# Kernel tuning notes

Hardware: AMD Instinct MI355X
Metric: run time of the kernel (lower is better)

The kernel has to match this reference:

```python
import jax, jax.numpy as jnp
import numpy as np
import math

B, T, WIDTH, NUM_HEADS, WINDOW = 2, 2048, 1024, 16, 1024
HEAD_DIM = WIDTH // NUM_HEADS
_MIN_LOGITS_VALUE = -1e30


def setup_inputs() -> dict:
    key = jax.random.key(0)
    k1, k2, k3, k4, k5 = jax.random.split(key, 5)
    std = math.sqrt(1.0 / WIDTH)
    x = jax.random.normal(k1, (B, T, WIDTH), dtype=jnp.float32)
    segment_pos = jnp.tile(jnp.arange(T, dtype=jnp.int32)[None, :], (B, 1))
    Wq = jax.random.normal(k2, (WIDTH, WIDTH), dtype=jnp.float32) * std
    Wk = jax.random.normal(k3, (HEAD_DIM, WIDTH), dtype=jnp.float32) * std
    Wv = jax.random.normal(k4, (HEAD_DIM, WIDTH), dtype=jnp.float32) * std
    Wf = jax.random.normal(k5, (WIDTH, WIDTH), dtype=jnp.float32) * std
    bf = jnp.zeros((WIDTH,), dtype=jnp.float32)
    return {"x": x, "segment_pos": segment_pos, "Wq": Wq, "Wk": Wk, "Wv": Wv, "Wf": Wf, "bf": bf}


def reference(x, segment_pos, Wq, Wk, Wv, Wf, bf):
    b, t, _ = x.shape
    # projections (torch Linear: y = x @ W.T)
    q = (x @ Wq.T).reshape(b, t, NUM_HEADS, HEAD_DIM)  # b t n h
    k = x @ Wk.T  # b s h  (single shared KV head, MQA)
    v = x @ Wv.T  # b s h
    scale = 1.0 / math.sqrt(HEAD_DIM)
    logits = jnp.einsum('btnh,bsh->bnts', q, k) * scale
    pos = jnp.arange(t)
    q_pos = pos[:, None]
    k_pos = pos[None, :]
    mask = (q_pos >= k_pos) & (q_pos <= k_pos + WINDOW)  # [t, t]
    masked = jnp.where(mask[None, None, :, :], logits, _MIN_LOGITS_VALUE)
    probs = jax.nn.softmax(masked.astype(jnp.float32), axis=-1).astype(logits.dtype)
    out = jnp.einsum('bnts,bsh->btnh', probs, v).reshape(b, t, WIDTH)
    return out @ Wf.T + bf
```

## Files before the change

kernel.cpp:

```cpp
#include <hip/hip_runtime.h>
#include <cstdint>
#include <cstddef>

#define BB      2
#define TT      2048
#define WID     1024
#define NH      16
#define HD      64
#define WIN     1024
#define MROWS   (BB*TT)
#define NQKV    1152
#define QSCL    0.18033688011112042f

typedef __attribute__((ext_vector_type(8))) short  short8;
typedef __attribute__((ext_vector_type(4))) float  floatx4;

__device__ __forceinline__ unsigned short f2bf(float f) {
  union { float f; unsigned int u; } v; v.f = f;
  unsigned int u = v.u;
  unsigned int r = (u + 0x7fffu + ((u >> 16) & 1u)) >> 16;
  return (unsigned short)r;
}

__device__ __forceinline__ float fast_exp2(float x) {
#if __has_builtin(__builtin_amdgcn_exp2f)
  return __builtin_amdgcn_exp2f(x);
#else
  return exp2f(x);
#endif
}

__device__ __forceinline__ unsigned int pk_bf16_trunc(float lo, float hi) {
  union { float f; unsigned int u; } a, b; a.f = lo; b.f = hi;
#if __has_builtin(__builtin_amdgcn_perm)
  return __builtin_amdgcn_perm(b.u, a.u, 0x07060302u);
#else
  return (b.u & 0xffff0000u) | (a.u >> 16);
#endif
}

__device__ __forceinline__ void gld_lds16(const void* g, void* l) {
  __builtin_amdgcn_global_load_lds(
      (const __attribute__((address_space(1))) unsigned int*)g,
      (__attribute__((address_space(3))) unsigned int*)l, 16, 0, 0);
}

__global__ __launch_bounds__(256) void convert_kernel(
    const float* __restrict__ x,  const float* __restrict__ wq,
    const float* __restrict__ wk, const float* __restrict__ wv,
    const float* __restrict__ wf,
    unsigned short* __restrict__ xb, unsigned short* __restrict__ wb,
    unsigned short* __restrict__ wfb)
{
  const int NX4 = (MROWS * WID) / 4;
  const int NQ4 = (WID * WID) / 4;
  const int NK4 = (HD * WID) / 4;
  const int NW4 = NQ4 + 2 * NK4;
  const int NF4 = (WID * WID) / 4;
  const int TOT = NX4 + NW4 + NF4;
  for (int i = blockIdx.x * blockDim.x + threadIdx.x; i < TOT;
       i += gridDim.x * blockDim.x) {
    float4 v4;
    unsigned short* dptr;
    if (i < NX4) {
      v4 = ((const float4*)x)[i];
      dptr = xb + (size_t)i * 4;
    } else if (i < NX4 + NW4) {
      int k = i - NX4;
      dptr = wb + (size_t)k * 4;
      if (k < NQ4)            v4 = ((const float4*)wq)[k];
      else if (k < NQ4 + NK4) v4 = ((const float4*)wk)[k - NQ4];
      else                    v4 = ((const float4*)wv)[k - NQ4 - NK4];
    } else {
      int k = i - NX4 - NW4;
      v4 = ((const float4*)wf)[k];
      dptr = wfb + (size_t)k * 4;
    }
    ushort4 o4 = make_ushort4(f2bf(v4.x), f2bf(v4.y), f2bf(v4.z), f2bf(v4.w));
    *(ushort4*)dptr = o4;
  }
}

__global__ __launch_bounds__(256) void gemm64(
    const unsigned short* __restrict__ A, const unsigned short* __restrict__ Bm,
    int M, int N, int K, int mode,
    float* __restrict__ C, const float* __restrict__ bias,
    unsigned short* __restrict__ qb, unsigned short* __restrict__ kb,
    unsigned short* __restrict__ vtb)
{
  __shared__ __align__(16) unsigned short As[2][64 * 64];
  __shared__ __align__(16) unsigned short Bs[2][128 * 64];

  const int tid  = threadIdx.x;
  const int m0   = blockIdx.x * 64;
  const int n0   = blockIdx.y * 128;
  const int w    = tid >> 6;
  const int lane = tid & 63;
  const int wr   = w >> 1;
  const int wc   = w & 1;
  const int quad = lane >> 4;
  const int l16  = lane & 15;

  const int rS  = tid >> 3;
  const int cS  = tid & 7;
  const int csS = (cS + rS) & 7;
  const unsigned short* gA0 = A  + (size_t)(m0 + rS) * K + csS * 8;
  const unsigned short* gA1 = gA0 + (size_t)32 * K;
  const unsigned short* gB0 = Bm + (size_t)(n0 + rS) * K + csS * 8;
  const unsigned short* gB1 = gB0 + (size_t)32 * K;
  const unsigned short* gB2 = gB0 + (size_t)64 * K;
  const unsigned short* gB3 = gB0 + (size_t)96 * K;
  const int wub = (tid & 192) * 16;

  floatx4 acc[2][4];
#pragma unroll
  for (int it = 0; it < 2; ++it)
#pragma unroll
    for (int jt = 0; jt < 4; ++jt)
      acc[it][jt] = (floatx4){0.f, 0.f, 0.f, 0.f};

  const int K64 = K >> 6;
  gld_lds16(gA0, (char*)As[0] + wub);
  gld_lds16(gA1, (char*)As[0] + 4096 + wub);
  gld_lds16(gB0, (char*)Bs[0] + wub);
  gld_lds16(gB1, (char*)Bs[0] + 4096 + wub);
  gld_lds16(gB2, (char*)Bs[0] + 8192 + wub);
  gld_lds16(gB3, (char*)Bs[0] + 12288 + wub);
  __syncthreads();

  for (int kt = 0; kt < K64; ++kt) {
    const int cur = kt & 1;
    if (kt + 1 < K64) {
      const int nxt = cur ^ 1;
      const int off = (kt + 1) * 64;
      gld_lds16(gA0 + off, (char*)As[nxt] + wub);
      gld_lds16(gA1 + off, (char*)As[nxt] + 4096 + wub);
      gld_lds16(gB0 + off, (char*)Bs[nxt] + wub);
      gld_lds16(gB1 + off, (char*)Bs[nxt] + 4096 + wub);
      gld_lds16(gB2 + off, (char*)Bs[nxt] + 8192 + wub);
      gld_lds16(gB3 + off, (char*)Bs[nxt] + 12288 + wub);
    }
    const unsigned short* as = As[cur];
    const unsigned short* bs = Bs[cur];
    short8 af[2][2], bfr[4][2];
#pragma unroll
    for (int it = 0; it < 2; ++it) {
      const int m = wr * 32 + it * 16 + l16;
#pragma unroll
      for (int ks = 0; ks < 2; ++ks)
        af[it][ks] = *(const short8*)(as + m * 64 + (((ks * 4 + quad) - m) & 7) * 8);
    }
#pragma unroll
    for (int jt = 0; jt < 4; ++jt) {
      const int n = wc * 64 + jt * 16 + l16;
#pragma unroll
      for (int ks = 0; ks < 2; ++ks)
        bfr[jt][ks] = *(const short8*)(bs + n * 64 + (((ks * 4 + quad) - n) & 7) * 8);
    }
#pragma unroll
    for (int ks = 0; ks < 2; ++ks)
#pragma unroll
      for (int it = 0; it < 2; ++it)
#pragma unroll
        for (int jt = 0; jt < 4; ++jt)
          acc[it][jt] = __builtin_amdgcn_mfma_f32_16x16x32_bf16(
              af[it][ks], bfr[jt][ks], acc[it][jt], 0, 0, 0);
    __syncthreads();
  }

  if (mode == 0) {
#pragma unroll
    for (int it = 0; it < 2; ++it) {
      const int gr = m0 + wr * 32 + it * 16 + quad * 4;
#pragma unroll
      for (int jt = 0; jt < 4; ++jt) {
        const int gc = n0 + wc * 64 + jt * 16 + l16;
        const float badd = bias[gc];
#pragma unroll
        for (int r = 0; r < 4; ++r)
          C[(size_t)(gr + r) * N + gc] = acc[it][jt][r] + badd;
      }
    }
  } else {
#pragma unroll
    for (int it = 0; it < 2; ++it) {
      const int gr = m0 + wr * 32 + it * 16 + quad * 4;
#pragma unroll
      for (int jt = 0; jt < 4; ++jt) {
        const int gc = n0 + wc * 64 + jt * 16 + l16;
        if (gc < WID) {
#pragma unroll
          for (int r = 0; r < 4; ++r)
            qb[(size_t)(gr + r) * WID + gc] = f2bf(acc[it][jt][r] * QSCL);
        } else if (gc < WID + HD) {
#pragma unroll
          for (int r = 0; r < 4; ++r)
            kb[(size_t)(gr + r) * HD + (gc - WID)] = f2bf(acc[it][jt][r]);
        } else {
          ushort4 o4 = make_ushort4(f2bf(acc[it][jt][0]), f2bf(acc[it][jt][1]),
                                    f2bf(acc[it][jt][2]), f2bf(acc[it][jt][3]));
          *(ushort4*)(vtb + (size_t)(gc - WID - HD) * MROWS + gr) = o4;
        }
      }
    }
  }
}

__global__ __launch_bounds__(512) void attn_mfma(
    const unsigned short* __restrict__ qb, const unsigned short* __restrict__ kb,
    const unsigned short* __restrict__ vtb, unsigned short* __restrict__ attnb)
{
  __shared__ __align__(16) unsigned short smem[30720];

  const int tid  = threadIdx.x;
  const int w    = tid >> 6;
  const int g    = w >> 2;
  const int wh   = w & 3;
  const int lane = tid & 63;
  const int l16  = lane & 15;
  const int quad = lane >> 4;
  const int t0   = blockIdx.x * 32;
  const int h    = blockIdx.y * 4 + wh;
  const int b    = blockIdx.z;

  unsigned short* Psb = smem + 20480 + w * 1280;

  short8 qf[2][2];
#pragma unroll
  for (int nt = 0; nt < 2; ++nt) {
    const unsigned short* qp =
        qb + (size_t)(b * TT + t0 + nt * 16 + l16) * WID + h * HD + quad * 8;
    qf[nt][0] = *(const short8*)qp;
    qf[nt][1] = *(const short8*)(qp + 32);
  }

  floatx4 Oacc[4][2];
#pragma unroll
  for (int mh = 0; mh < 4; ++mh)
#pragma unroll
    for (int nt = 0; nt < 2; ++nt)
      Oacc[mh][nt] = (floatx4){0.f, 0.f, 0.f, 0.f};
  float lq[2] = {0.f, 0.f};

  int s_begin = t0 - WIN; if (s_begin < 0) s_begin = 0;
  const int T = ((t0 + 32) - s_begin) >> 5;
  const int I = (T + 1) >> 1;

  const int kkey  = tid >> 3;
  const int khseg = (tid & 7) * 8;
  const int ksel  = kkey >> 5, krow = kkey & 31;
  const int vhd   = tid >> 3;
  const int vkk   = (tid & 7) * 8;
  const int vsel  = vkk >> 5,  vcol = vkk & 31;

  const unsigned short* kbase = kb  + (size_t)(b * TT) * HD;
  const unsigned short* vbase = vtb + (size_t)vhd * MROWS + b * TT;

  int s0p = s_begin;
  int ck = s0p + kkey; if (ck > TT - 1) ck = TT - 1;
  int cv = s0p + vkk;  if (cv > TT - 8) cv = TT - 8;
  short8 kreg = *(const short8*)(kbase + (size_t)ck * HD + khseg);
  short8 vreg = *(const short8*)(vbase + cv);

  for (int i = 0; i < I; ++i) {
    const int buf = i & 1;
    *(short8*)(smem + buf * 5120 + ksel * 2560 + krow * 80 + khseg) = kreg;
    *(short8*)(smem + 10240 + buf * 5120 + vsel * 2560 + vhd * 40 + vcol) = vreg;
    __syncthreads();
    if (i + 1 < I) {
      s0p += 64;
      ck = s0p + kkey; if (ck > TT - 1) ck = TT - 1;
      cv = s0p + vkk;  if (cv > TT - 8) cv = TT - 8;
      kreg = *(const short8*)(kbase + (size_t)ck * HD + khseg);
      vreg = *(const short8*)(vbase + cv);
    }

    const int ta = 2 * i + g;
    if (ta < T) {
      const int s0 = s_begin + ta * 32;
      const unsigned short* ks = smem + buf * 5120 + g * 2560;
      const unsigned short* vs = smem + 10240 + buf * 5120 + g * 2560;

      short8 kf[2][2];
#pragma unroll
      for (int mk = 0; mk < 2; ++mk)
#pragma unroll
        for (int k2 = 0; k2 < 2; ++k2)
          kf[mk][k2] = *(const short8*)(ks + (mk * 16 + l16) * 80 + k2 * 32 + quad * 8);

      floatx4 Sc[2][2];
#pragma unroll
      for (int mk = 0; mk < 2; ++mk)
#pragma unroll
        for (int nt = 0; nt < 2; ++nt)
          Sc[mk][nt] = (floatx4){0.f, 0.f, 0.f, 0.f};
#pragma unroll
      for (int mk = 0; mk < 2; ++mk)
#pragma unroll
        for (int nt = 0; nt < 2; ++nt)
#pragma unroll
          for (int k2 = 0; k2 < 2; ++k2)
            Sc[mk][nt] = __builtin_amdgcn_mfma_f32_16x16x32_bf16(
                kf[mk][k2], qf[nt][k2], Sc[mk][nt], 0, 0, 0);

      const int mode = (s0 == t0) ? 2 : ((t0 >= WIN && s0 == t0 - WIN) ? 1 : 0);

#pragma unroll
      for (int nt = 0; nt < 2; ++nt) {
        const int t = t0 + nt * 16 + l16;
        float p[8], ps = 0.f;
#pragma unroll
        for (int mk = 0; mk < 2; ++mk)
#pragma unroll
          for (int r = 0; r < 4; ++r) {
            float v = Sc[mk][nt][r];
            if (mode) {
              const int s = s0 + mk * 16 + quad * 4 + r;
              const bool kill = (mode == 2) ? (s > t) : (s + WIN < t);
              if (kill) v = -1.0e5f;
            }
            const float e = fast_exp2(v);
            p[mk * 4 + r] = e; ps += e;
          }
        lq[nt] += ps;
        uint2 w0 = make_uint2(pk_bf16_trunc(p[0], p[1]), pk_bf16_trunc(p[2], p[3]));
        uint2 w1 = make_uint2(pk_bf16_trunc(p[4], p[5]), pk_bf16_trunc(p[6], p[7]));
        *(uint2*)(Psb + (nt * 16 + l16) * 40 + quad * 4)      = w0;
        *(uint2*)(Psb + (nt * 16 + l16) * 40 + 16 + quad * 4) = w1;
      }

      short8 pf0 = *(const short8*)(Psb + l16 * 40 + quad * 8);
      short8 pf1 = *(const short8*)(Psb + (16 + l16) * 40 + quad * 8);
#pragma unroll
      for (int mh = 0; mh < 4; ++mh) {
        short8 vf = *(const short8*)(vs + (mh * 16 + l16) * 40 + quad * 8);
        Oacc[mh][0] = __builtin_amdgcn_mfma_f32_16x16x32_bf16(vf, pf0, Oacc[mh][0], 0, 0, 0);
        Oacc[mh][1] = __builtin_amdgcn_mfma_f32_16x16x32_bf16(vf, pf1, Oacc[mh][1], 0, 0, 0);
      }
    }
  }

  lq[0] += __shfl_xor(lq[0], 16); lq[0] += __shfl_xor(lq[0], 32);
  lq[1] += __shfl_xor(lq[1], 16); lq[1] += __shfl_xor(lq[1], 32);

  __syncthreads();
  float* mrg = (float*)smem;
  float* ob  = mrg + wh * 2336 + lane * 36;
  if (g == 1) {
#pragma unroll
    for (int mh = 0; mh < 4; ++mh)
#pragma unroll
      for (int nt = 0; nt < 2; ++nt)
        *(floatx4*)(ob + mh * 8 + nt * 4) = Oacc[mh][nt];
    if (quad == 0) {
      mrg[wh * 2336 + 2304 + l16]      = lq[0];
      mrg[wh * 2336 + 2304 + 16 + l16] = lq[1];
    }
  }
  __syncthreads();
  if (g == 0) {
    lq[0] += mrg[wh * 2336 + 2304 + l16];
    lq[1] += mrg[wh * 2336 + 2304 + 16 + l16];
#pragma unroll
    for (int nt = 0; nt < 2; ++nt) {
      const float inv = 1.f / lq[nt];
      unsigned short* op = attnb + (size_t)(b * TT + t0 + nt * 16 + l16) * WID
                         + h * HD + quad * 4;
#pragma unroll
      for (int mh = 0; mh < 4; ++mh) {
        floatx4 o1 = *(const floatx4*)(ob + mh * 8 + nt * 4);
        ushort4 o4 = make_ushort4(f2bf((Oacc[mh][nt][0] + o1[0]) * inv),
                                  f2bf((Oacc[mh][nt][1] + o1[1]) * inv),
                                  f2bf((Oacc[mh][nt][2] + o1[2]) * inv),
                                  f2bf((Oacc[mh][nt][3] + o1[3]) * inv));
        *(ushort4*)(op + mh * 16) = o4;
      }
    }
  }
}

extern "C" void kernel_launch(void* const* d_in, const int* in_sizes, int n_in,
                              void* d_out, int out_size, void* d_ws, size_t ws_size,
                              hipStream_t stream) {
  const float* x   = (const float*)d_in[0];
  const float* wq  = (const float*)d_in[2];
  const float* wk  = (const float*)d_in[3];
  const float* wv  = (const float*)d_in[4];
  const float* wf  = (const float*)d_in[5];
  const float* bfp = (const float*)d_in[6];
  float* out = (float*)d_out;

  char* ws = (char*)d_ws;
  unsigned short* xb   = (unsigned short*)(ws + 0);
  unsigned short* wb   = (unsigned short*)(ws + 8388608);
  unsigned short* wfb  = (unsigned short*)(ws + 10747904);
  unsigned short* qbuf = (unsigned short*)(ws + 12845056);
  unsigned short* kbuf = (unsigned short*)(ws + 21233664);
  unsigned short* vtb  = (unsigned short*)(ws + 21757952);
  unsigned short* attnb = xb;

  hipLaunchKernelGGL(convert_kernel, dim3(1024), dim3(256), 0, stream,
                     x, wq, wk, wv, wf, xb, wb, wfb);
  hipLaunchKernelGGL(gemm64, dim3(MROWS / 64, NQKV / 128), dim3(256), 0, stream,
                     xb, wb, MROWS, NQKV, WID, 1,
                     (float*)nullptr, (const float*)nullptr, qbuf, kbuf, vtb);
  hipLaunchKernelGGL(attn_mfma, dim3(TT / 32, NH / 4, BB), dim3(512), 0, stream,
                     qbuf, kbuf, vtb, attnb);
  hipLaunchKernelGGL(gemm64, dim3(MROWS / 64, WID / 128), dim3(256), 0, stream,
                     attnb, wfb, MROWS, WID, WID, 0,
                     out, bfp, (unsigned short*)nullptr, (unsigned short*)nullptr,
                     (unsigned short*)nullptr);
}
```

Measured before the change: 150.8 us.

## Load K/V fragments directly from global memory and shrink attention blocks

The attention kernel no longer stages K and V tiles through double-buffered shared memory with block-wide barriers. Each wave now reads its K and V MFMA fragments straight from global memory, relying on L1/L2 caching because all heads share the single MQA KV head. Blocks shrink from 8 to 4 waves covering 2 heads, and the smaller LDS footprint lets more blocks fit per CU. The cost is redundant global/L2 traffic for K/V across waves and blocks, plus loss of the explicit prefetch overlap.

```diff
diff --git a/kernel.cpp b/kernel.cpp
--- a/kernel.cpp
+++ b/kernel.cpp
@@ -206,24 +206,24 @@
   }
 }
 
-__global__ __launch_bounds__(512) void attn_mfma(
+__global__ __launch_bounds__(256, 4) void attn_mfma(
     const unsigned short* __restrict__ qb, const unsigned short* __restrict__ kb,
     const unsigned short* __restrict__ vtb, unsigned short* __restrict__ attnb)
 {
-  __shared__ __align__(16) unsigned short smem[30720];
+  __shared__ __align__(16) unsigned short smem[9472];
 
   const int tid  = threadIdx.x;
   const int w    = tid >> 6;
-  const int g    = w >> 2;
-  const int wh   = w & 3;
+  const int g    = w >> 1;
+  const int wh   = w & 1;
   const int lane = tid & 63;
   const int l16  = lane & 15;
   const int quad = lane >> 4;
   const int t0   = blockIdx.x * 32;
-  const int h    = blockIdx.y * 4 + wh;
+  const int h    = blockIdx.y * 2 + wh;
   const int b    = blockIdx.z;
 
-  unsigned short* Psb = smem + 20480 + w * 1280;
+  unsigned short* Psb = smem + w * 1280;
 
   short8 qf[2][2];
 #pragma unroll
@@ -244,99 +244,73 @@
 
   int s_begin = t0 - WIN; if (s_begin < 0) s_begin = 0;
   const int T = ((t0 + 32) - s_begin) >> 5;
-  const int I = (T + 1) >> 1;
-
-  const int kkey  = tid >> 3;
-  const int khseg = (tid & 7) * 8;
-  const int ksel  = kkey >> 5, krow = kkey & 31;
-  const int vhd   = tid >> 3;
-  const int vkk   = (tid & 7) * 8;
-  const int vsel  = vkk >> 5,  vcol = vkk & 31;
-
-  const unsigned short* kbase = kb  + (size_t)(b * TT) * HD;
-  const unsigned short* vbase = vtb + (size_t)vhd * MROWS + b * TT;
-
-  int s0p = s_begin;
-  int ck = s0p + kkey; if (ck > TT - 1) ck = TT - 1;
-  int cv = s0p + vkk;  if (cv > TT - 8) cv = TT - 8;
-  short8 kreg = *(const short8*)(kbase + (size_t)ck * HD + khseg);
-  short8 vreg = *(const short8*)(vbase + cv);
-
-  for (int i = 0; i < I; ++i) {
-    const int buf = i & 1;
-    *(short8*)(smem + buf * 5120 + ksel * 2560 + krow * 80 + khseg) = kreg;
-    *(short8*)(smem + 10240 + buf * 5120 + vsel * 2560 + vhd * 40 + vcol) = vreg;
-    __syncthreads();
-    if (i + 1 < I) {
-      s0p += 64;
-      ck = s0p + kkey; if (ck > TT - 1) ck = TT - 1;
-      cv = s0p + vkk;  if (cv > TT - 8) cv = TT - 8;
-      kreg = *(const short8*)(kbase + (size_t)ck * HD + khseg);
-      vreg = *(const short8*)(vbase + cv);
-    }
-
-    const int ta = 2 * i + g;
-    if (ta < T) {
-      const int s0 = s_begin + ta * 32;
-      const unsigned short* ks = smem + buf * 5120 + g * 2560;
-      const unsigned short* vs = smem + 10240 + buf * 5120 + g * 2560;
-
-      short8 kf[2][2];
+
+  const unsigned short* kB = kb  + (size_t)(b * TT) * HD;
+
+  for (int ta = g; ta < T; ta += 2) {
+    const int s0 = s_begin + ta * 32;
+
+    short8 kf[2][2];
+#pragma unroll
+    for (int mk = 0; mk < 2; ++mk) {
+      const unsigned short* kp = kB + (size_t)(s0 + mk * 16 + l16) * HD + quad * 8;
+      kf[mk][0] = *(const short8*)kp;
+      kf[mk][1] = *(const short8*)(kp + 32);
+    }
+
+    floatx4 Sc[2][2];
+#pragma unroll
+    for (int mk = 0; mk < 2; ++mk)
+#pragma unroll
+      for (int nt = 0; nt < 2; ++nt)
+        Sc[mk][nt] = (floatx4){0.f, 0.f, 0.f, 0.f};
+#pragma unroll
+    for (int mk = 0; mk < 2; ++mk)
+#pragma unroll
+      for (int nt = 0; nt < 2; ++nt)
+#pragma unroll
+        for (int k2 = 0; k2 < 2; ++k2)
+          Sc[mk][nt] = __builtin_amdgcn_mfma_f32_16x16x32_bf16(
+              kf[mk][k2], qf[nt][k2], Sc[mk][nt], 0, 0, 0);
+
+    short8 vf[4];
+#pragma unroll
+    for (int mh = 0; mh < 4; ++mh)
+      vf[mh] = *(const short8*)(vtb + (size_t)(mh * 16 + l16) * MROWS
+                                + b * TT + s0 + quad * 8);
+
+    const int mode = (s0 == t0) ? 2 : ((t0 >= WIN && s0 == t0 - WIN) ? 1 : 0);
+
+#pragma unroll
+    for (int nt = 0; nt < 2; ++nt) {
+      const int t = t0 + nt * 16 + l16;
+      float p[8], ps = 0.f;
 #pragma unroll
       for (int mk = 0; mk < 2; ++mk)
 #pragma unroll
-        for (int k2 = 0; k2 < 2; ++k2)
-          kf[mk][k2] = *(const short8*)(ks + (mk * 16 + l16) * 80 + k2 * 32 + quad * 8);
-
-      floatx4 Sc[2][2];
-#pragma unroll
-      for (int mk = 0; mk < 2; ++mk)
-#pragma unroll
-        for (int nt = 0; nt < 2; ++nt)
-          Sc[mk][nt] = (floatx4){0.f, 0.f, 0.f, 0.f};
-#pragma unroll
-      for (int mk = 0; mk < 2; ++mk)
-#pragma unroll
-        for (int nt = 0; nt < 2; ++nt)
-#pragma unroll
-          for (int k2 = 0; k2 < 2; ++k2)
-            Sc[mk][nt] = __builtin_amdgcn_mfma_f32_16x16x32_bf16(
-                kf[mk][k2], qf[nt][k2], Sc[mk][nt], 0, 0, 0);
-
-      const int mode = (s0 == t0) ? 2 : ((t0 >= WIN && s0 == t0 - WIN) ? 1 : 0);
-
-#pragma unroll
-      for (int nt = 0; nt < 2; ++nt) {
-        const int t = t0 + nt * 16 + l16;
-        float p[8], ps = 0.f;
-#pragma unroll
-        for (int mk = 0; mk < 2; ++mk)
-#pragma unroll
-          for (int r = 0; r < 4; ++r) {
-            float v = Sc[mk][nt][r];
-            if (mode) {
-              const int s = s0 + mk * 16 + quad * 4 + r;
-              const bool kill = (mode == 2) ? (s > t) : (s + WIN < t);
-              if (kill) v = -1.0e5f;
-            }
-            const float e = fast_exp2(v);
-            p[mk * 4 + r] = e; ps += e;
+        for (int r = 0; r < 4; ++r) {
+          float v = Sc[mk][nt][r];
+          if (mode) {
+            const int s = s0 + mk * 16 + quad * 4 + r;
+            const bool kill = (mode == 2) ? (s > t) : (s + WIN < t);
+            if (kill) v = -1.0e5f;
           }
-        lq[nt] += ps;
-        uint2 w0 = make_uint2(pk_bf16_trunc(p[0], p[1]), pk_bf16_trunc(p[2], p[3]));
-        uint2 w1 = make_uint2(pk_bf16_trunc(p[4], p[5]), pk_bf16_trunc(p[6], p[7]));
-        *(uint2*)(Psb + (nt * 16 + l16) * 40 + quad * 4)      = w0;
-        *(uint2*)(Psb + (nt * 16 + l16) * 40 + 16 + quad * 4) = w1;
-      }
-
-      short8 pf0 = *(const short8*)(Psb + l16 * 40 + quad * 8);
-      short8 pf1 = *(const short8*)(Psb + (16 + l16) * 40 + quad * 8);
-#pragma unroll
-      for (int mh = 0; mh < 4; ++mh) {
-        short8 vf = *(const short8*)(vs + (mh * 16 + l16) * 40 + quad * 8);
-        Oacc[mh][0] = __builtin_amdgcn_mfma_f32_16x16x32_bf16(vf, pf0, Oacc[mh][0], 0, 0, 0);
-        Oacc[mh][1] = __builtin_amdgcn_mfma_f32_16x16x32_bf16(vf, pf1, Oacc[mh][1], 0, 0, 0);
-      }
+          const float e = fast_exp2(v);
+          p[mk * 4 + r] = e; ps += e;
+        }
+      lq[nt] += ps;
+      uint2 w0 = make_uint2(pk_bf16_trunc(p[0], p[1]), pk_bf16_trunc(p[2], p[3]));
+      uint2 w1 = make_uint2(pk_bf16_trunc(p[4], p[5]), pk_bf16_trunc(p[6], p[7]));
+      *(uint2*)(Psb + (nt * 16 + l16) * 40 + quad * 4)      = w0;
+      *(uint2*)(Psb + (nt * 16 + l16) * 40 + 16 + quad * 4) = w1;
+    }
+
+    short8 pf0 = *(const short8*)(Psb + l16 * 40 + quad * 8);
+    short8 pf1 = *(const short8*)(Psb + (16 + l16) * 40 + quad * 8);
+#pragma unroll
+    for (int mh = 0; mh < 4; ++mh) {
+      Oacc[mh][0] = __builtin_amdgcn_mfma_f32_16x16x32_bf16(vf[mh], pf0, Oacc[mh][0], 0, 0, 0);
+      Oacc[mh][1] = __builtin_amdgcn_mfma_f32_16x16x32_bf16(vf[mh], pf1, Oacc[mh][1], 0, 0, 0);
     }
   }
 
@@ -345,7 +319,7 @@
 
   __syncthreads();
   float* mrg = (float*)smem;
-  float* ob  = mrg + wh * 2336 + lane * 36;
+  float* ob  = mrg + wh * 2304 + lane * 36;
   if (g == 1) {
 #pragma unroll
     for (int mh = 0; mh < 4; ++mh)
@@ -353,14 +327,14 @@
       for (int nt = 0; nt < 2; ++nt)
         *(floatx4*)(ob + mh * 8 + nt * 4) = Oacc[mh][nt];
     if (quad == 0) {
-      mrg[wh * 2336 + 2304 + l16]      = lq[0];
-      mrg[wh * 2336 + 2304 + 16 + l16] = lq[1];
+      mrg[4608 + wh * 32 + l16]      = lq[0];
+      mrg[4608 + wh * 32 + 16 + l16] = lq[1];
     }
   }
   __syncthreads();
   if (g == 0) {
-    lq[0] += mrg[wh * 2336 + 2304 + l16];
-    lq[1] += mrg[wh * 2336 + 2304 + 16 + l16];
+    lq[0] += mrg[4608 + wh * 32 + l16];
+    lq[1] += mrg[4608 + wh * 32 + 16 + l16];
 #pragma unroll
     for (int nt = 0; nt < 2; ++nt) {
       const float inv = 1.f / lq[nt];
@@ -404,7 +378,7 @@
   hipLaunchKernelGGL(gemm64, dim3(MROWS / 64, NQKV / 128), dim3(256), 0, stream,
                      xb, wb, MROWS, NQKV, WID, 1,
                      (float*)nullptr, (const float*)nullptr, qbuf, kbuf, vtb);
-  hipLaunchKernelGGL(attn_mfma, dim3(TT / 32, NH / 4, BB), dim3(512), 0, stream,
+  hipLaunchKernelGGL(attn_mfma, dim3(TT / 32, NH / 2, BB), dim3(256), 0, stream,
                      qbuf, kbuf, vtb, attnb);
   hipLaunchKernelGGL(gemm64, dim3(MROWS / 64, WID / 128), dim3(256), 0, stream,
                      attnb, wfb, MROWS, WID, WID, 0,
```

Result: slower. 182.8 us (+21.2%).

## Split-K the projection GEMMs into two partials and add combine kernels

Applied to the files above, without the earlier changes.

Both GEMMs now split K into two halves across blockIdx.z and write fp32 partial results to a workspace buffer. Separate combine kernels then sum the partials and apply the Q scale, bf16 conversion, V transpose and output bias. The goal is more blocks and better CU occupancy on the large GPU. The cost is extra fp32 traffic for the partial results (about 38 MB for QKV and 33 MB for the output) and two extra kernel launches.

```diff
diff --git a/kernel.cpp b/kernel.cpp
--- a/kernel.cpp
+++ b/kernel.cpp
@@ -81,12 +81,9 @@
   }
 }
 
-__global__ __launch_bounds__(256) void gemm64(
+__global__ __launch_bounds__(256) void gemm64s(
     const unsigned short* __restrict__ A, const unsigned short* __restrict__ Bm,
-    int M, int N, int K, int mode,
-    float* __restrict__ C, const float* __restrict__ bias,
-    unsigned short* __restrict__ qb, unsigned short* __restrict__ kb,
-    unsigned short* __restrict__ vtb)
+    float* __restrict__ P, int M, int N, int K)
 {
   __shared__ __align__(16) unsigned short As[2][64 * 64];
   __shared__ __align__(16) unsigned short Bs[2][128 * 64];
@@ -94,6 +91,9 @@
   const int tid  = threadIdx.x;
   const int m0   = blockIdx.x * 64;
   const int n0   = blockIdx.y * 128;
+  const int part = blockIdx.z;
+  const int Ks   = K >> 1;
+  const int kb0  = part * Ks;
   const int w    = tid >> 6;
   const int lane = tid & 63;
   const int wr   = w >> 1;
@@ -104,9 +104,9 @@
   const int rS  = tid >> 3;
   const int cS  = tid & 7;
   const int csS = (cS + rS) & 7;
-  const unsigned short* gA0 = A  + (size_t)(m0 + rS) * K + csS * 8;
+  const unsigned short* gA0 = A  + (size_t)(m0 + rS) * K + kb0 + csS * 8;
   const unsigned short* gA1 = gA0 + (size_t)32 * K;
-  const unsigned short* gB0 = Bm + (size_t)(n0 + rS) * K + csS * 8;
+  const unsigned short* gB0 = Bm + (size_t)(n0 + rS) * K + kb0 + csS * 8;
   const unsigned short* gB1 = gB0 + (size_t)32 * K;
   const unsigned short* gB2 = gB0 + (size_t)64 * K;
   const unsigned short* gB3 = gB0 + (size_t)96 * K;
@@ -119,7 +119,7 @@
     for (int jt = 0; jt < 4; ++jt)
       acc[it][jt] = (floatx4){0.f, 0.f, 0.f, 0.f};
 
-  const int K64 = K >> 6;
+  const int K64 = Ks >> 6;
   gld_lds16(gA0, (char*)As[0] + wub);
   gld_lds16(gA1, (char*)As[0] + 4096 + wub);
   gld_lds16(gB0, (char*)Bs[0] + wub);
@@ -168,41 +168,81 @@
     __syncthreads();
   }
 
-  if (mode == 0) {
-#pragma unroll
-    for (int it = 0; it < 2; ++it) {
-      const int gr = m0 + wr * 32 + it * 16 + quad * 4;
-#pragma unroll
-      for (int jt = 0; jt < 4; ++jt) {
-        const int gc = n0 + wc * 64 + jt * 16 + l16;
-        const float badd = bias[gc];
-#pragma unroll
-        for (int r = 0; r < 4; ++r)
-          C[(size_t)(gr + r) * N + gc] = acc[it][jt][r] + badd;
-      }
-    }
-  } else {
-#pragma unroll
-    for (int it = 0; it < 2; ++it) {
-      const int gr = m0 + wr * 32 + it * 16 + quad * 4;
-#pragma unroll
-      for (int jt = 0; jt < 4; ++jt) {
-        const int gc = n0 + wc * 64 + jt * 16 + l16;
-        if (gc < WID) {
-#pragma unroll
-          for (int r = 0; r < 4; ++r)
-            qb[(size_t)(gr + r) * WID + gc] = f2bf(acc[it][jt][r] * QSCL);
-        } else if (gc < WID + HD) {
-#pragma unroll
-          for (int r = 0; r < 4; ++r)
-            kb[(size_t)(gr + r) * HD + (gc - WID)] = f2bf(acc[it][jt][r]);
-        } else {
-          ushort4 o4 = make_ushort4(f2bf(acc[it][jt][0]), f2bf(acc[it][jt][1]),
-                                    f2bf(acc[it][jt][2]), f2bf(acc[it][jt][3]));
-          *(ushort4*)(vtb + (size_t)(gc - WID - HD) * MROWS + gr) = o4;
-        }
-      }
-    }
+  float* Pp = P + (size_t)part * M * N;
+#pragma unroll
+  for (int it = 0; it < 2; ++it) {
+    const int gr = m0 + wr * 32 + it * 16 + quad * 4;
+#pragma unroll
+    for (int jt = 0; jt < 4; ++jt) {
+      const int gc = n0 + wc * 64 + jt * 16 + l16;
+#pragma unroll
+      for (int r = 0; r < 4; ++r)
+        Pp[(size_t)(gr + r) * N + gc] = acc[it][jt][r];
+    }
+  }
+}
+
+__global__ __launch_bounds__(256) void combine_qkv(
+    const float* __restrict__ P, unsigned short* __restrict__ qb,
+    unsigned short* __restrict__ kb, unsigned short* __restrict__ vtb)
+{
+  const float* P0 = P;
+  const float* P1 = P + (size_t)MROWS * NQKV;
+  const int NQ4 = MROWS * WID / 4;
+  const int NK4 = MROWS * HD / 4;
+  const int NV  = HD * (MROWS / 4);
+  const int TOT = NQ4 + NK4 + NV;
+  for (int i = blockIdx.x * blockDim.x + threadIdx.x; i < TOT;
+       i += gridDim.x * blockDim.x) {
+    if (i < NQ4) {
+      const int row = i >> 8;
+      const int c   = (i & 255) << 2;
+      const float4 a = *(const float4*)(P0 + (size_t)row * NQKV + c);
+      const float4 b = *(const float4*)(P1 + (size_t)row * NQKV + c);
+      ushort4 o = make_ushort4(f2bf((a.x + b.x) * QSCL), f2bf((a.y + b.y) * QSCL),
+                               f2bf((a.z + b.z) * QSCL), f2bf((a.w + b.w) * QSCL));
+      *(ushort4*)(qb + (size_t)row * WID + c) = o;
+    } else if (i < NQ4 + NK4) {
+      const int j   = i - NQ4;
+      const int row = j >> 4;
+      const int c   = (j & 15) << 2;
+      const float4 a = *(const float4*)(P0 + (size_t)row * NQKV + WID + c);
+      const float4 b = *(const float4*)(P1 + (size_t)row * NQKV + WID + c);
+      ushort4 o = make_ushort4(f2bf(a.x + b.x), f2bf(a.y + b.y),
+                               f2bf(a.z + b.z), f2bf(a.w + b.w));
+      *(ushort4*)(kb + (size_t)row * HD + c) = o;
+    } else {
+      const int j  = i - NQ4 - NK4;
+      const int hd = j >> 10;
+      const int r4 = (j & 1023) << 2;
+      const int col = WID + HD + hd;
+      ushort4 o;
+      o.x = f2bf(P0[(size_t)(r4 + 0) * NQKV + col] + P1[(size_t)(r4 + 0) * NQKV + col]);
+      o.y = f2bf(P0[(size_t)(r4 + 1) * NQKV + col] + P1[(size_t)(r4 + 1) * NQKV + col]);
+      o.z = f2bf(P0[(size_t)(r4 + 2) * NQKV + col] + P1[(size_t)(r4 + 2) * NQKV + col]);
+      o.w = f2bf(P0[(size_t)(r4 + 3) * NQKV + col] + P1[(size_t)(r4 + 3) * NQKV + col]);
+      *(ushort4*)(vtb + (size_t)hd * MROWS + r4) = o;
+    }
+  }
+}
+
+__global__ __launch_bounds__(256) void combine_out(
+    const float* __restrict__ P, const float* __restrict__ bias,
+    float* __restrict__ out)
+{
+  const float* P0 = P;
+  const float* P1 = P + (size_t)MROWS * WID;
+  const int TOT = MROWS * WID / 4;
+  for (int i = blockIdx.x * blockDim.x + threadIdx.x; i < TOT;
+       i += gridDim.x * blockDim.x) {
+    const int c = (i & 255) << 2;
+    const float4 a  = ((const float4*)P0)[i];
+    const float4 b  = ((const float4*)P1)[i];
+    const float4 bs = *(const float4*)(bias + c);
+    float4 o;
+    o.x = a.x + b.x + bs.x; o.y = a.y + b.y + bs.y;
+    o.z = a.z + b.z + bs.z; o.w = a.w + b.w + bs.w;
+    ((float4*)out)[i] = o;
   }
 }
 
@@ -397,17 +437,19 @@
   unsigned short* qbuf = (unsigned short*)(ws + 12845056);
   unsigned short* kbuf = (unsigned short*)(ws + 21233664);
   unsigned short* vtb  = (unsigned short*)(ws + 21757952);
+  float*          pbuf = (float*)(ws + 22282240);
   unsigned short* attnb = xb;
 
   hipLaunchKernelGGL(convert_kernel, dim3(1024), dim3(256), 0, stream,
                      x, wq, wk, wv, wf, xb, wb, wfb);
-  hipLaunchKernelGGL(gemm64, dim3(MROWS / 64, NQKV / 128), dim3(256), 0, stream,
-                     xb, wb, MROWS, NQKV, WID, 1,
-                     (float*)nullptr, (const float*)nullptr, qbuf, kbuf, vtb);
+  hipLaunchKernelGGL(gemm64s, dim3(MROWS / 64, NQKV / 128, 2), dim3(256), 0, stream,
+                     xb, wb, pbuf, MROWS, NQKV, WID);
+  hipLaunchKernelGGL(combine_qkv, dim3(2048), dim3(256), 0, stream,
+                     pbuf, qbuf, kbuf, vtb);
   hipLaunchKernelGGL(attn_mfma, dim3(TT / 32, NH / 4, BB), dim3(512), 0, stream,
                      qbuf, kbuf, vtb, attnb);
-  hipLaunchKernelGGL(gemm64, dim3(MROWS / 64, WID / 128), dim3(256), 0, stream,
-                     attnb, wfb, MROWS, WID, WID, 0,
-                     out, bfp, (unsigned short*)nullptr, (unsigned short*)nullptr,
-                     (unsigned short*)nullptr);
-}
+  hipLaunchKernelGGL(gemm64s, dim3(MROWS / 64, WID / 128, 2), dim3(256), 0, stream,
+                     attnb, wfb, pbuf, MROWS, WID, WID);
+  hipLaunchKernelGGL(combine_out, dim3(2048), dim3(256), 0, stream,
+                     pbuf, bfp, out);
+}
```

After: 172.5 us. +14.4%, slower.
